# Kernel tuning notes

Measured on AMD Instinct MI355X. Metric: run time of the kernel, lower is better.

Reference implementation:

```python
import jax, jax.numpy as jnp
import numpy as np

B = 16384
N_NARR = 128
N_SUB = 1024
K = N_SUB // N_NARR  # narrative i -> subnarratives [i*K, (i+1)*K)
GAMMA = 2.0
NW, SW, HW = 1.0, 1.0, 0.5  # narrative/subnarrative/hierarchy weights


def setup_inputs() -> dict:
    key = jax.random.key(0)
    k1, k2, k3, k4 = jax.random.split(key, 4)
    return {
        "narrative_logits": jax.random.normal(k1, (B, N_NARR), jnp.float32),
        "subnarrative_logits": jax.random.normal(k2, (B, N_SUB), jnp.float32),
        "narrative_labels": jax.random.randint(k3, (B, N_NARR), 0, 2, jnp.int32),
        "subnarrative_labels": jax.random.randint(k4, (B, N_SUB), 0, 2, jnp.int32),
    }


def _weighted_bce(logits, labels, pos_weight):
    # BCEWithLogits with pos_weight: pw*y*softplus(-x) + (1-y)*softplus(x)
    return pos_weight * labels * jax.nn.softplus(-logits) + (1.0 - labels) * jax.nn.softplus(logits)


def reference(narrative_logits, subnarrative_logits, narrative_labels, subnarrative_labels):
    nl = narrative_labels.astype(jnp.float32)
    sl = subnarrative_labels.astype(jnp.float32)
    b = narrative_logits.shape[0]

    # class-balanced pos_weights, clamped to [1, 50]
    npw = jnp.clip((1.0 - nl).sum(0) / (nl.sum(0) + 1e-6), 1.0, 50.0)
    spw = jnp.clip((1.0 - sl).sum(0) / (sl.sum(0) + 1e-6), 1.0, 50.0)

    narrative_loss = _weighted_bce(narrative_logits, nl, npw).mean()

    # ragged subnarrative loss, vectorized: groups of K subnarrs per narrative.
    # per-(sample, positive-narrative) mean BCE over the group, averaged over
    # the number of valid (sample, narrative) pairs -- same math as the loop.
    sub_bce = _weighted_bce(subnarrative_logits, sl, spw).reshape(b, N_NARR, K)
    per_group = sub_bce.mean(-1)              # [B, N_NARR]
    pos = nl                                   # positive-narrative mask [B, N_NARR]
    valid_count = pos.sum()
    subnarrative_loss = jnp.where(
        valid_count > 0, (per_group * pos).sum() / jnp.maximum(valid_count, 1.0), 0.0)

    # hierarchy consistency: relu(max subnarr prob - narr prob) over positives
    nprob = jax.nn.sigmoid(narrative_logits)
    sprob = jax.nn.sigmoid(subnarrative_logits)
    grp_max = sprob.reshape(b, N_NARR, K).max(-1)  # [B, N_NARR]
    hierarchy_loss = (jax.nn.relu(grp_max - nprob) * pos).sum() / b

    # focal terms (mean over all elements)
    nf = ((1.0 - nprob) ** GAMMA * nl * jax.nn.log_sigmoid(narrative_logits)).mean()
    sf = ((1.0 - sprob) ** GAMMA * sl * jax.nn.log_sigmoid(subnarrative_logits)).mean()

    total = (NW * (narrative_loss - 0.1 * nf)
             + SW * (subnarrative_loss - 0.1 * sf)
             + HW * hierarchy_loss)
    return total
```

## Files before the change

kernel.cpp:

```cpp
#include <hip/hip_runtime.h>


#define BDIM 256
#define NROWS 16384
#define NNARR 128
#define NSUB 1024
#define RPB 16
#define NBLOCKS (NROWS / RPB)

#define WS_AN    0
#define WS_CN    128
#define WS_NSUM  256
#define WS_AS    384
#define WS_CS    1408
#define WS_SSUM  2432
#define WS_FN    3456
#define WS_FS    3457
#define WS_HIER  3458
#define WS_FLOATS 3459
#define CSTRIDE  3472

#define NCHUNK 16
#define TPG (NBLOCKS / NCHUNK)

__device__ __forceinline__ void bce_pieces(float x, float& sp_p, float& sp_m, float& sig) {
    float a = fabsf(x);
    float e = __expf(-a);
    float l = __logf(1.0f + e);
    sp_p = fmaxf(x, 0.0f) + l;
    sp_m = sp_p - x;
    float inv = __builtin_amdgcn_rcpf(1.0f + e);
    sig = (x >= 0.0f) ? inv : e * inv;
}

#define ROW_BODY(xs, ys, nx, posv)                                            \
  {                                                                           \
    float nsp_p, nsp_m, nsig;                                                 \
    bce_pieces((nx), nsp_p, nsp_m, nsig);                                     \
    const float xv0 = (xs).x, xv1 = (xs).y, xv2 = (xs).z, xv3 = (xs).w;       \
    const float yv0 = (float)(ys).x, yv1 = (float)(ys).y,                     \
                yv2 = (float)(ys).z, yv3 = (float)(ys).w;                     \
    float mymax = 0.0f;                                                       \
    {                                                                         \
      float sp_p, sp_m, sig;                                                  \
      bce_pieces(xv0, sp_p, sp_m, sig);                                       \
      As[0] += (posv) * yv0 * sp_m;                                           \
      Cs[0] += (posv) * (1.0f - yv0) * sp_p;                                  \
      ss[0] += yv0;                                                           \
      float om = 1.0f - sig;                                                  \
      fs += om * om * yv0 * (-sp_m);                                          \
      mymax = fmaxf(mymax, sig);                                              \
    }                                                                         \
    {                                                                         \
      float sp_p, sp_m, sig;                                                  \
      bce_pieces(xv1, sp_p, sp_m, sig);                                       \
      As[1] += (posv) * yv1 * sp_m;                                           \
      Cs[1] += (posv) * (1.0f - yv1) * sp_p;                                  \
      ss[1] += yv1;                                                           \
      float om = 1.0f - sig;                                                  \
      fs += om * om * yv1 * (-sp_m);                                          \
      mymax = fmaxf(mymax, sig);                                              \
    }                                                                         \
    {                                                                         \
      float sp_p, sp_m, sig;                                                  \
      bce_pieces(xv2, sp_p, sp_m, sig);                                       \
      As[2] += (posv) * yv2 * sp_m;                                           \
      Cs[2] += (posv) * (1.0f - yv2) * sp_p;                                  \
      ss[2] += yv2;                                                           \
      float om = 1.0f - sig;                                                  \
      fs += om * om * yv2 * (-sp_m);                                          \
      mymax = fmaxf(mymax, sig);                                              \
    }                                                                         \
    {                                                                         \
      float sp_p, sp_m, sig;                                                  \
      bce_pieces(xv3, sp_p, sp_m, sig);                                       \
      As[3] += (posv) * yv3 * sp_m;                                           \
      Cs[3] += (posv) * (1.0f - yv3) * sp_p;                                  \
      ss[3] += yv3;                                                           \
      float om = 1.0f - sig;                                                  \
      fs += om * om * yv3 * (-sp_m);                                          \
      mymax = fmaxf(mymax, sig);                                              \
    }                                                                         \
    float gmax = fmaxf(mymax, __shfl_xor(mymax, 1, 64));                      \
    if ((t & 1) == 0) {                                                       \
        hier += fmaxf(gmax - nsig, 0.0f) * (posv);                            \
        An += (posv) * nsp_m;                                                 \
        Cn += (1.0f - (posv)) * nsp_p;                                        \
        ns += (posv);                                                         \
        float om = 1.0f - nsig;                                               \
        fn += om * om * (posv) * (-nsp_m);                                    \
    }                                                                         \
  }

__global__ void __launch_bounds__(BDIM)
__attribute__((amdgpu_waves_per_eu(4, 4)))
ncl_main(
    const float* __restrict__ nlog, const float* __restrict__ slog,
    const int*   __restrict__ nlab, const int*   __restrict__ slab,
    float* __restrict__ P)
{
    __shared__ float ssc[4][3];

    const int t  = threadIdx.x;
    const int g  = t >> 1;
    const int r0 = blockIdx.x * RPB;
    float* const Pb = P + (size_t)blockIdx.x * CSTRIDE;

    float As[4] = {0,0,0,0}, Cs[4] = {0,0,0,0}, ss[4] = {0,0,0,0};
    float An = 0.f, Cn = 0.f, ns = 0.f, fn = 0.f, fs = 0.f, hier = 0.f;

    const float* sp = slog + (size_t)r0 * NSUB + 4 * t;
    const int*   lp = slab + (size_t)r0 * NSUB + 4 * t;
    const float* np = nlog + (size_t)r0 * NNARR + g;
    const int*   mp = nlab + (size_t)r0 * NNARR + g;

    #pragma unroll 1
    for (int i = 0; i < RPB; i += 2) {
        const float4 xsA = *(const float4*)(sp + (size_t)i * NSUB);
        const int4   ysA = *(const int4*)  (lp + (size_t)i * NSUB);
        const float  nxA = np[(size_t)i * NNARR];
        const float  pvA = (float)mp[(size_t)i * NNARR];
        const float4 xsB = *(const float4*)(sp + (size_t)(i + 1) * NSUB);
        const int4   ysB = *(const int4*)  (lp + (size_t)(i + 1) * NSUB);
        const float  nxB = np[(size_t)(i + 1) * NNARR];
        const float  pvB = (float)mp[(size_t)(i + 1) * NNARR];

        ROW_BODY(xsA, ysA, nxA, pvA);
        ROW_BODY(xsB, ysB, nxB, pvB);
    }

    *(float4*)(Pb + WS_AS   + 4 * t) = make_float4(As[0], As[1], As[2], As[3]);
    *(float4*)(Pb + WS_CS   + 4 * t) = make_float4(Cs[0], Cs[1], Cs[2], Cs[3]);
    *(float4*)(Pb + WS_SSUM + 4 * t) = make_float4(ss[0], ss[1], ss[2], ss[3]);
    if ((t & 1) == 0) {
        Pb[WS_AN   + g] = An;
        Pb[WS_CN   + g] = Cn;
        Pb[WS_NSUM + g] = ns;
    }

    #pragma unroll
    for (int off = 32; off; off >>= 1) {
        fn   += __shfl_down(fn,   off, 64);
        fs   += __shfl_down(fs,   off, 64);
        hier += __shfl_down(hier, off, 64);
    }
    if ((t & 63) == 0) {
        int w = t >> 6;
        ssc[w][0] = fn; ssc[w][1] = fs; ssc[w][2] = hier;
    }
    __syncthreads();
    if (t == 0) {
        float a = 0.f, b = 0.f, c = 0.f;
        #pragma unroll
        for (int w = 0; w < 4; ++w) { a += ssc[w][0]; b += ssc[w][1]; c += ssc[w][2]; }
        Pb[WS_FN] = a; Pb[WS_FS] = b; Pb[WS_HIER] = c;
    }
}

__global__ __launch_bounds__(256) void ncl_reduce1(const float* __restrict__ P,
                                                   float* __restrict__ tmp)
{
    const int e = blockIdx.x * 256 + threadIdx.x;
    if (e >= WS_FLOATS) return;
    const int gg = blockIdx.y;
    const float* p = P + (size_t)gg * TPG * CSTRIDE + e;
    float s = 0.f;
    #pragma unroll 4
    for (int i = 0; i < TPG; ++i)
        s += p[(size_t)i * CSTRIDE];
    tmp[(size_t)gg * CSTRIDE + e] = s;
}

__global__ __launch_bounds__(1024) void ncl_finalize(const float* __restrict__ tmp,
                                                     float* __restrict__ out)
{
    __shared__ float sr[6][16];
    const int t = threadIdx.x;
    const float Bf = (float)NROWS;

    float As = 0.f, Csv = 0.f, ss = 0.f;
    #pragma unroll 4
    for (int gc = 0; gc < NCHUNK; ++gc) {
        const float* p = tmp + (size_t)gc * CSTRIDE;
        As  += p[WS_AS   + t];
        Csv += p[WS_CS   + t];
        ss  += p[WS_SSUM + t];
    }
    float spw = fminf(fmaxf((Bf - ss) / (ss + 1e-6f), 1.0f), 50.0f);
    float sub_part = spw * As + Csv;

    float narr_part = 0.f, valid_part = 0.f;
    if (t < NNARR) {
        float An = 0.f, Cn = 0.f, ns = 0.f;
        #pragma unroll 4
        for (int gc = 0; gc < NCHUNK; ++gc) {
            const float* p = tmp + (size_t)gc * CSTRIDE;
            An += p[WS_AN + t]; Cn += p[WS_CN + t]; ns += p[WS_NSUM + t];
        }
        float npw = fminf(fmaxf((Bf - ns) / (ns + 1e-6f), 1.0f), 50.0f);
        narr_part  = npw * An + Cn;
        valid_part = ns;
    }

    float fn_p = 0.f, fs_p = 0.f, hier_p = 0.f;
    if (t < NCHUNK) {
        const float* p = tmp + (size_t)t * CSTRIDE;
        fn_p = p[WS_FN]; fs_p = p[WS_FS]; hier_p = p[WS_HIER];
    }

    #pragma unroll
    for (int off = 32; off; off >>= 1) {
        sub_part   += __shfl_down(sub_part,   off, 64);
        narr_part  += __shfl_down(narr_part,  off, 64);
        valid_part += __shfl_down(valid_part, off, 64);
        fn_p       += __shfl_down(fn_p,       off, 64);
        fs_p       += __shfl_down(fs_p,       off, 64);
        hier_p     += __shfl_down(hier_p,     off, 64);
    }
    if ((t & 63) == 0) {
        int w = t >> 6;
        sr[0][w] = sub_part; sr[1][w] = narr_part; sr[2][w] = valid_part;
        sr[3][w] = fn_p;     sr[4][w] = fs_p;      sr[5][w] = hier_p;
    }
    __syncthreads();
    if (t == 0) {
        float sub_tot = 0.f, narr_tot = 0.f, valid = 0.f;
        float fn = 0.f, fs = 0.f, hier = 0.f;
        #pragma unroll
        for (int i = 0; i < 16; ++i) {
            sub_tot += sr[0][i]; narr_tot += sr[1][i]; valid += sr[2][i];
            fn += sr[3][i]; fs += sr[4][i]; hier += sr[5][i];
        }

        float narrative_loss = narr_tot / (Bf * (float)NNARR);
        float sub_loss = (valid > 0.0f) ? (sub_tot * (1.0f / 8.0f)) / fmaxf(valid, 1.0f) : 0.0f;
        float nf = fn / (Bf * (float)NNARR);
        float sf = fs / (Bf * (float)NSUB);
        float hier_loss = hier / Bf;

        out[0] = (narrative_loss - 0.1f * nf)
               + (sub_loss       - 0.1f * sf)
               + 0.5f * hier_loss;
    }
}

extern "C" void kernel_launch(void* const* d_in, const int* in_sizes, int n_in,
                              void* d_out, int out_size, void* d_ws, size_t ws_size,
                              hipStream_t stream) {
    const float* nlog = (const float*)d_in[0];
    const float* slog = (const float*)d_in[1];
    const int*   nlab = (const int*)d_in[2];
    const int*   slab = (const int*)d_in[3];
    float* P   = (float*)d_ws;
    float* tmp = P + (size_t)NBLOCKS * CSTRIDE;
    float* out = (float*)d_out;

    ncl_main<<<NBLOCKS, BDIM, 0, stream>>>(nlog, slog, nlab, slab, P);
    dim3 gr((WS_FLOATS + 255) / 256, NCHUNK);
    ncl_reduce1<<<gr, 256, 0, stream>>>(P, tmp);
    ncl_finalize<<<1, 1024, 0, stream>>>(tmp, out);
}
```

Baseline: 182.2 us.

## Stage subnarrative tiles through LDS with double-buffered async global_load_lds

Replaces the direct per-thread float4/int4 register loads of subnarrative logits and labels with asynchronous global-to-LDS copies into a two-stage buffer. The next 4-row tile is prefetched while the current tile is computed, aiming to hide memory latency. It also drops the waves_per_eu attribute. The 64 KB of shared memory per block cuts how many blocks fit on a CU, and each tile still ends with a full vmcnt wait, so less latency may be hidden than before.

```diff
diff --git a/kernel.cpp b/kernel.cpp
--- a/kernel.cpp
+++ b/kernel.cpp
@@ -7,6 +7,8 @@
 #define NSUB 1024
 #define RPB 16
 #define NBLOCKS (NROWS / RPB)
+#define TROWS 4
+#define NT (RPB / TROWS)
 
 #define WS_AN    0
 #define WS_CN    128
@@ -23,6 +25,13 @@
 #define NCHUNK 16
 #define TPG (NBLOCKS / NCHUNK)
 
+typedef __attribute__((address_space(1))) const unsigned int as1_u32;
+typedef __attribute__((address_space(3))) unsigned int as3_u32;
+
+__device__ __forceinline__ void load16_lds(const void* g, void* l) {
+    __builtin_amdgcn_global_load_lds((as1_u32*)g, (as3_u32*)l, 16, 0, 0);
+}
+
 __device__ __forceinline__ void bce_pieces(float x, float& sp_p, float& sp_m, float& sig) {
     float a = fabsf(x);
     float e = __expf(-a);
@@ -92,13 +101,37 @@
     }                                                                         \
   }
 
-__global__ void __launch_bounds__(BDIM)
-__attribute__((amdgpu_waves_per_eu(4, 4)))
-ncl_main(
+#define STAGE(buf, tile)                                                      \
+  {                                                                           \
+    const int rbase = r0 + (tile) * TROWS;                                    \
+    _Pragma("unroll")                                                         \
+    for (int rr = 0; rr < TROWS; ++rr) {                                      \
+      const size_t roff = (size_t)(rbase + rr) * NSUB + 4 * (size_t)t;        \
+      load16_lds(slog + roff, &ls_x[buf][rr][(t >> 6) << 8]);                 \
+      load16_lds(slab + roff, &ls_y[buf][rr][(t >> 6) << 8]);                 \
+    }                                                                         \
+  }
+
+#define COMPUTE(buf, tile)                                                    \
+  {                                                                           \
+    _Pragma("unroll")                                                         \
+    for (int rr = 0; rr < TROWS; ++rr) {                                      \
+      const int r = r0 + (tile) * TROWS + rr;                                 \
+      const float4 xs = *(const float4*)&ls_x[buf][rr][4 * t];                \
+      const int4   ys = *(const int4*)  &ls_y[buf][rr][4 * t];                \
+      const float  nx   = nlog[(size_t)r * NNARR + g];                        \
+      const float  posv = (float)nlab[(size_t)r * NNARR + g];                 \
+      ROW_BODY(xs, ys, nx, posv);                                             \
+    }                                                                         \
+  }
+
+__global__ __launch_bounds__(BDIM) void ncl_main(
     const float* __restrict__ nlog, const float* __restrict__ slog,
     const int*   __restrict__ nlab, const int*   __restrict__ slab,
     float* __restrict__ P)
 {
+    __shared__ float ls_x[2][TROWS][NSUB];
+    __shared__ int   ls_y[2][TROWS][NSUB];
     __shared__ float ssc[4][3];
 
     const int t  = threadIdx.x;
@@ -109,24 +142,16 @@
     float As[4] = {0,0,0,0}, Cs[4] = {0,0,0,0}, ss[4] = {0,0,0,0};
     float An = 0.f, Cn = 0.f, ns = 0.f, fn = 0.f, fs = 0.f, hier = 0.f;
 
-    const float* sp = slog + (size_t)r0 * NSUB + 4 * t;
-    const int*   lp = slab + (size_t)r0 * NSUB + 4 * t;
-    const float* np = nlog + (size_t)r0 * NNARR + g;
-    const int*   mp = nlab + (size_t)r0 * NNARR + g;
-
-    #pragma unroll 1
-    for (int i = 0; i < RPB; i += 2) {
-        const float4 xsA = *(const float4*)(sp + (size_t)i * NSUB);
-        const int4   ysA = *(const int4*)  (lp + (size_t)i * NSUB);
-        const float  nxA = np[(size_t)i * NNARR];
-        const float  pvA = (float)mp[(size_t)i * NNARR];
-        const float4 xsB = *(const float4*)(sp + (size_t)(i + 1) * NSUB);
-        const int4   ysB = *(const int4*)  (lp + (size_t)(i + 1) * NSUB);
-        const float  nxB = np[(size_t)(i + 1) * NNARR];
-        const float  pvB = (float)mp[(size_t)(i + 1) * NNARR];
-
-        ROW_BODY(xsA, ysA, nxA, pvA);
-        ROW_BODY(xsB, ysB, nxB, pvB);
+    STAGE(0, 0);
+    asm volatile("s_waitcnt vmcnt(0)" ::: "memory");
+
+    #pragma unroll
+    for (int tile = 0; tile < NT; ++tile) {
+        const int cb = tile & 1;
+        if (tile + 1 < NT) STAGE(cb ^ 1, tile + 1);
+        COMPUTE(cb, tile);
+        if (tile + 1 < NT)
+            asm volatile("s_waitcnt vmcnt(0)" ::: "memory");
     }
 
     *(float4*)(Pb + WS_AS   + 4 * t) = make_float4(As[0], As[1], As[2], As[3]);
```

After: 227.3 us. 1.25x slower.
